# Kernel tuning notes

Measured on AMD Instinct MI355X. Metric: run time of the kernel, lower is better.

## Reference

```python
import jax, jax.numpy as jnp
import numpy as np

FEAT = 1152
HID = [768, 512, 256]
WS = 32
LN_EPS = 1e-5


def _ln(x, g, b):
    mu = jnp.mean(x, axis=-1, keepdims=True)
    var = jnp.mean(jnp.square(x - mu), axis=-1, keepdims=True)
    return (x - mu) * jax.lax.rsqrt(var + LN_EPS) * g + b


def setup_inputs() -> dict:
    key = jax.random.key(0)
    ks = jax.random.split(key, 16)
    B, N, C = 8, 9216, FEAT

    def lin(k, din, dout):
        s = 1.0 / np.sqrt(din)
        k1, k2 = jax.random.split(k)
        return (jax.random.uniform(k1, (din, dout), jnp.float32, -s, s),
                jax.random.uniform(k2, (dout,), jnp.float32, -s, s))

    x = jax.random.normal(ks[0], (B, N, C), jnp.float32)
    W1, b1 = lin(ks[1], C, HID[0])
    W2, b2 = lin(ks[2], HID[0], HID[1])
    W3, b3 = lin(ks[3], HID[1], HID[2])
    Wo, bo = lin(ks[4], HID[2], C)
    red = C // 8
    ca_w1, ca_b1 = lin(ks[5], C, red)
    ca_w2, ca_b2 = lin(ks[6], red, C)
    return {
        "x": x,
        "W1": W1, "b1": b1, "g1": jnp.ones((HID[0],)), "be1": jnp.zeros((HID[0],)),
        "W2": W2, "b2": b2, "g2": jnp.ones((HID[1],)), "be2": jnp.zeros((HID[1],)),
        "W3": W3, "b3": b3, "g3": jnp.ones((HID[2],)), "be3": jnp.zeros((HID[2],)),
        "Wo": Wo, "bo": bo,
        "ca_w1": ca_w1, "ca_b1": ca_b1, "ca_w2": ca_w2, "ca_b2": ca_b2,
    }


def reference(x, W1, b1, g1, be1, W2, b2, g2, be2, W3, b3, g3, be3,
              Wo, bo, ca_w1, ca_b1, ca_w2, ca_b2):
    B, N, C = x.shape
    # projection + hidden blocks: Linear -> GELU(exact) -> LayerNorm
    h = _ln(jax.nn.gelu(x @ W1 + b1, approximate=False), g1, be1)
    h = _ln(jax.nn.gelu(h @ W2 + b2, approximate=False), g2, be2)
    h = _ln(jax.nn.gelu(h @ W3 + b3, approximate=False), g3, be3)
    y = h @ Wo + bo  # (B, N, C)
    # SE channel attention: global avg-pool over seq, 1x1 convs (=linear)
    pooled = jnp.mean(y, axis=1)                                  # (B, C)
    s = jax.nn.relu(pooled @ ca_w1 + ca_b1)                       # (B, C/8)
    s = jax.nn.sigmoid(s @ ca_w2 + ca_b2)                         # (B, C)
    y = y * s[:, None, :]
    # block-diagonal local self-attention, window = WS, scale 1/sqrt(C)
    nw = N // WS
    yw = y.reshape(B, nw, WS, C)
    scores = jnp.einsum('bwqc,bwkc->bwqk', yw, yw) / jnp.sqrt(jnp.asarray(C, y.dtype))
    attn = jax.nn.softmax(scores, axis=-1)
    out = jnp.einsum('bwqk,bwkc->bwqc', attn, yw)
    return out.reshape(B, N, C)
```

## Files before the change

### kernel.cpp

```cpp
#include <hip/hip_runtime.h>
#include <cstdint>
#include <cstddef>

typedef __bf16 bf16;
typedef __bf16 bf16x8 __attribute__((ext_vector_type(8)));
typedef float f32x4 __attribute__((ext_vector_type(4)));

__device__ __forceinline__ void gload_lds16(const bf16* g, bf16* l) {
    __builtin_amdgcn_global_load_lds((const __attribute__((address_space(1))) void*)g,
                                     (__attribute__((address_space(3))) void*)l, 16, 0, 0);
}

__global__ void cvt_f32_bf16_kernel(const float* __restrict__ in, bf16* __restrict__ outp, size_t n) {
    const size_t i = ((size_t)blockIdx.x * 256 + threadIdx.x) * 8;
    if (i >= n) return;
    const float4 a = *(const float4*)(in + i);
    const float4 b = *(const float4*)(in + i + 4);
    bf16x8 o;
    o[0] = (bf16)a.x; o[1] = (bf16)a.y; o[2] = (bf16)a.z; o[3] = (bf16)a.w;
    o[4] = (bf16)b.x; o[5] = (bf16)b.y; o[6] = (bf16)b.z; o[7] = (bf16)b.w;
    *(bf16x8*)(outp + i) = o;
}

__global__ void wtrans_all_kernel(const float* __restrict__ W1, bf16* __restrict__ T1,
                                  const float* __restrict__ W2, bf16* __restrict__ T2,
                                  const float* __restrict__ W3, bf16* __restrict__ T3,
                                  const float* __restrict__ Wo, bf16* __restrict__ To)
{
    __shared__ bf16 tile[64][65];
    const int id = blockIdx.x;
    const int t = threadIdx.x;
    const float* W; bf16* T; int K, N, kb, nb;
    if (id < 216)      { W = W1; T = T1; K = 1152; N = 768;  const int r = id;       kb = r % 18; nb = r / 18; }
    else if (id < 312) { W = W2; T = T2; K = 768;  N = 512;  const int r = id - 216; kb = r % 12; nb = r / 12; }
    else if (id < 344) { W = W3; T = T3; K = 512;  N = 256;  const int r = id - 312; kb = r % 8;  nb = r / 8;  }
    else               { W = Wo; T = To; K = 256;  N = 1152; const int r = id - 344; kb = r % 4;  nb = r / 4;  }
    const int k0 = kb << 6;
    const int n0 = nb << 6;
#pragma unroll
    for (int i = 0; i < 16; ++i) {
        const int flat = i * 256 + t;
        const int r = flat >> 6;
        const int c = flat & 63;
        tile[c][r] = (bf16)W[(size_t)(k0 + r) * N + n0 + c];
    }
    __syncthreads();
#pragma unroll
    for (int i = 0; i < 16; ++i) {
        const int flat = i * 256 + t;
        const int r = flat >> 6;
        const int c = flat & 63;
        T[(size_t)(n0 + r) * K + k0 + c] = tile[r][c];
    }
}

__device__ __forceinline__ int xcd_swz(int bid, int nwg) {
    return (bid & 7) * (nwg >> 3) + (bid >> 3);
}

__global__ void gemm_bf16_kernel(const bf16* __restrict__ A, const bf16* __restrict__ Bt,
                                 const float* __restrict__ bias, bf16* __restrict__ C,
                                 int K, int N, int nx, int do_gelu,
                                 float* __restrict__ ppart)
{
    __shared__ bf16 Alds[128 * 64];
    __shared__ bf16 Blds[128 * 64];
    __shared__ float psum[2][128];
    const int t = threadIdx.x;
    const int w = t >> 6;
    const int l = t & 63;
    const int l15 = l & 15, l4 = l >> 4;
    const int wgid = xcd_swz(blockIdx.x, gridDim.x);
    const int mblk = wgid / nx;
    const int nblk = wgid - mblk * nx;
    const int m0 = mblk << 7;
    const int n0 = nblk << 7;
    const int wm = (w >> 1) << 6;
    const int wn = (w & 1) << 6;

    f32x4 acc[4][4] = {};

    int sr[4], sg[4];
#pragma unroll
    for (int i = 0; i < 4; ++i) {
        const int flat = i * 256 + t;
        sr[i] = flat >> 3;
        sg[i] = ((flat & 7) ^ (sr[i] & 7)) << 3;
    }

    for (int k0 = 0; k0 < K; k0 += 64) {
#pragma unroll
        for (int i = 0; i < 4; ++i) {
            gload_lds16(A + (size_t)(m0 + sr[i]) * K + (k0 + sg[i]),
                        &Alds[(size_t)(i * 256 + (w << 6)) << 3]);
            gload_lds16(Bt + (size_t)(n0 + sr[i]) * K + (k0 + sg[i]),
                        &Blds[(size_t)(i * 256 + (w << 6)) << 3]);
        }
        __syncthreads();
#pragma unroll
        for (int kk = 0; kk < 2; ++kk) {
            bf16x8 af[4], bfv[4];
#pragma unroll
            for (int i = 0; i < 4; ++i) {
                const int r = wm + (i << 4) + l15;
                const int g = (kk << 2) + l4;
                af[i] = *(const bf16x8*)&Alds[(r << 6) + ((g ^ (r & 7)) << 3)];
                const int rn = wn + (i << 4) + l15;
                bfv[i] = *(const bf16x8*)&Blds[(rn << 6) + ((g ^ (rn & 7)) << 3)];
            }
#pragma unroll
            for (int i = 0; i < 4; ++i)
#pragma unroll
                for (int j = 0; j < 4; ++j)
                    acc[i][j] = __builtin_amdgcn_mfma_f32_16x16x32_bf16(af[i], bfv[j], acc[i][j], 0, 0, 0);
        }
        __syncthreads();
    }

#pragma unroll
    for (int i = 0; i < 4; ++i) {
        const int mb = m0 + wm + (i << 4) + (l4 << 2);
#pragma unroll
        for (int j = 0; j < 4; ++j) {
            const int col = n0 + wn + (j << 4) + l15;
            const float bv = bias[col];
#pragma unroll
            for (int r = 0; r < 4; ++r) {
                float v = acc[i][j][r] + bv;
                if (do_gelu) v = 0.5f * v * (1.0f + erff(v * 0.70710678118654752f));
                C[(size_t)(mb + r) * N + col] = (bf16)v;
            }
        }
    }

    if (ppart) {
#pragma unroll
        for (int j = 0; j < 4; ++j) {
            float cs = 0.f;
#pragma unroll
            for (int i = 0; i < 4; ++i)
#pragma unroll
                for (int r = 0; r < 4; ++r) cs += acc[i][j][r];
            cs += __shfl_xor(cs, 16, 64);
            cs += __shfl_xor(cs, 32, 64);
            if (l4 == 0) psum[w >> 1][((w & 1) << 6) + (j << 4) + l15] = cs;
        }
        __syncthreads();
        if (t < 128) {
            const int col = n0 + t;
            ppart[(size_t)mblk * N + col] = psum[0][t] + psum[1][t] + 128.0f * bias[col];
        }
    }
}

__global__ void ln768_kernel(bf16* __restrict__ H, const float* __restrict__ g,
                             const float* __restrict__ be)
{
    const int t = threadIdx.x;
    const int rloc = t >> 7;
    const int u = t & 127;
    bf16* hp = H + ((size_t)blockIdx.x * 2 + rloc) * 768;
    float v[8];
    float s1 = 0.f, s2 = 0.f;
    if (u < 96) {
        const bf16x8 hv = *(const bf16x8*)(hp + u * 8);
#pragma unroll
        for (int e = 0; e < 8; ++e) { v[e] = (float)hv[e]; s1 += v[e]; s2 += v[e] * v[e]; }
    }
#pragma unroll
    for (int m = 1; m < 64; m <<= 1) { s1 += __shfl_xor(s1, m, 64); s2 += __shfl_xor(s2, m, 64); }
    __shared__ float red[8];
    const int w = t >> 6;
    if ((t & 63) == 0) { red[w] = s1; red[w + 4] = s2; }
    __syncthreads();
    const int wb = rloc << 1;
    s1 = red[wb] + red[wb + 1];
    s2 = red[wb + 4] + red[wb + 5];
    const float mu = s1 * (1.0f / 768.0f);
    const float rstd = rsqrtf(s2 * (1.0f / 768.0f) - mu * mu + 1e-5f);
    if (u < 96) {
        const float4 g0 = *(const float4*)(g + u * 8);
        const float4 g1 = *(const float4*)(g + u * 8 + 4);
        const float4 b0 = *(const float4*)(be + u * 8);
        const float4 b1 = *(const float4*)(be + u * 8 + 4);
        bf16x8 o;
        o[0] = (bf16)((v[0] - mu) * rstd * g0.x + b0.x);
        o[1] = (bf16)((v[1] - mu) * rstd * g0.y + b0.y);
        o[2] = (bf16)((v[2] - mu) * rstd * g0.z + b0.z);
        o[3] = (bf16)((v[3] - mu) * rstd * g0.w + b0.w);
        o[4] = (bf16)((v[4] - mu) * rstd * g1.x + b1.x);
        o[5] = (bf16)((v[5] - mu) * rstd * g1.y + b1.y);
        o[6] = (bf16)((v[6] - mu) * rstd * g1.z + b1.z);
        o[7] = (bf16)((v[7] - mu) * rstd * g1.w + b1.w);
        *(bf16x8*)(hp + u * 8) = o;
    }
}

__global__ void ln512_kernel(bf16* __restrict__ H, const float* __restrict__ g,
                             const float* __restrict__ be)
{
    const int t = threadIdx.x;
    const int w = t >> 6, l = t & 63;
    bf16* hp = H + ((size_t)blockIdx.x * 4 + w) * 512;
    const bf16x8 hv = *(const bf16x8*)(hp + l * 8);
    float v[8];
    float s1 = 0.f, s2 = 0.f;
#pragma unroll
    for (int e = 0; e < 8; ++e) { v[e] = (float)hv[e]; s1 += v[e]; s2 += v[e] * v[e]; }
#pragma unroll
    for (int m = 1; m < 64; m <<= 1) { s1 += __shfl_xor(s1, m, 64); s2 += __shfl_xor(s2, m, 64); }
    const float mu = s1 * (1.0f / 512.0f);
    const float rstd = rsqrtf(s2 * (1.0f / 512.0f) - mu * mu + 1e-5f);
    const float4 g0 = *(const float4*)(g + l * 8);
    const float4 g1 = *(const float4*)(g + l * 8 + 4);
    const float4 b0 = *(const float4*)(be + l * 8);
    const float4 b1 = *(const float4*)(be + l * 8 + 4);
    bf16x8 o;
    o[0] = (bf16)((v[0] - mu) * rstd * g0.x + b0.x);
    o[1] = (bf16)((v[1] - mu) * rstd * g0.y + b0.y);
    o[2] = (bf16)((v[2] - mu) * rstd * g0.z + b0.z);
    o[3] = (bf16)((v[3] - mu) * rstd * g0.w + b0.w);
    o[4] = (bf16)((v[4] - mu) * rstd * g1.x + b1.x);
    o[5] = (bf16)((v[5] - mu) * rstd * g1.y + b1.y);
    o[6] = (bf16)((v[6] - mu) * rstd * g1.z + b1.z);
    o[7] = (bf16)((v[7] - mu) * rstd * g1.w + b1.w);
    *(bf16x8*)(hp + l * 8) = o;
}

__global__ void ln256_kernel(bf16* __restrict__ H, const float* __restrict__ g,
                             const float* __restrict__ be)
{
    const int t = threadIdx.x;
    const int rloc = t >> 5, l = t & 31;
    bf16* hp = H + ((size_t)blockIdx.x * 8 + rloc) * 256;
    const bf16x8 hv = *(const bf16x8*)(hp + l * 8);
    float v[8];
    float s1 = 0.f, s2 = 0.f;
#pragma unroll
    for (int e = 0; e < 8; ++e) { v[e] = (float)hv[e]; s1 += v[e]; s2 += v[e] * v[e]; }
#pragma unroll
    for (int m = 1; m < 32; m <<= 1) { s1 += __shfl_xor(s1, m, 64); s2 += __shfl_xor(s2, m, 64); }
    const float mu = s1 * (1.0f / 256.0f);
    const float rstd = rsqrtf(s2 * (1.0f / 256.0f) - mu * mu + 1e-5f);
    const float4 g0 = *(const float4*)(g + l * 8);
    const float4 g1 = *(const float4*)(g + l * 8 + 4);
    const float4 b0 = *(const float4*)(be + l * 8);
    const float4 b1 = *(const float4*)(be + l * 8 + 4);
    bf16x8 o;
    o[0] = (bf16)((v[0] - mu) * rstd * g0.x + b0.x);
    o[1] = (bf16)((v[1] - mu) * rstd * g0.y + b0.y);
    o[2] = (bf16)((v[2] - mu) * rstd * g0.z + b0.z);
    o[3] = (bf16)((v[3] - mu) * rstd * g0.w + b0.w);
    o[4] = (bf16)((v[4] - mu) * rstd * g1.x + b1.x);
    o[5] = (bf16)((v[5] - mu) * rstd * g1.y + b1.y);
    o[6] = (bf16)((v[6] - mu) * rstd * g1.z + b1.z);
    o[7] = (bf16)((v[7] - mu) * rstd * g1.w + b1.w);
    *(bf16x8*)(hp + l * 8) = o;
}

__global__ void se_kernel(const float* __restrict__ ppart,
                          const float* __restrict__ w1, const float* __restrict__ b1,
                          const float* __restrict__ w2, const float* __restrict__ b2,
                          float* __restrict__ sbuf)
{
    const int b = blockIdx.x, t = threadIdx.x;
    __shared__ float p[1152];
    __shared__ float t1[144];
    for (int c = t; c < 1152; c += 256) {
        float s = 0.f;
#pragma unroll 8
        for (int j = 0; j < 72; ++j) s += ppart[(size_t)(b * 72 + j) * 1152 + c];
        p[c] = s * (1.0f / 9216.0f);
    }
    __syncthreads();
    if (t < 144) {
        float a = b1[t];
        for (int k = 0; k < 1152; ++k) a += p[k] * w1[k * 144 + t];
        t1[t] = a > 0.f ? a : 0.f;
    }
    __syncthreads();
    for (int c = t; c < 1152; c += 256) {
        float a = b2[c];
#pragma unroll 8
        for (int k = 0; k < 144; ++k) a += t1[k] * w2[k * 1152 + c];
        sbuf[b * 1152 + c] = 1.0f / (1.0f + expf(-a));
    }
}

__device__ __forceinline__ int fswz(int r) { return (r & 7) ^ ((r >> 3) & 3); }

#define OSTG_STRIDE 388

__global__ void attn_kernel(const bf16* __restrict__ Y, const float* __restrict__ sbuf,
                            float* __restrict__ out)
{
    __shared__ __align__(16) char smem[24576 + 24832 + 2048];
    bf16*  yw   = (bf16*)smem;
    float* SpF  = (float*)(smem + 24576);
    float* ostg = (float*)(smem + 24576);
    bf16*  P    = (bf16*)(smem + 24576 + 24832);

    const int t = threadIdx.x;
    const int w = t >> 6, l = t & 63;
    const int l15 = l & 15, l4 = l >> 4;
    const int wdx = blockIdx.x, b = blockIdx.y;

    const bf16* Yp = Y + ((size_t)b * 9216 + (size_t)wdx * 32) * 1152;
    const float* sv = sbuf + b * 1152;
    float* op = out + ((size_t)b * 9216 + (size_t)wdx * 32) * 1152;

    auto stage_chunk = [&](int cc) {
#pragma unroll
        for (int i = 0; i < 6; ++i) {
            const int flat = i * 256 + t;
            const int r = flat / 48;
            const int gg = flat - r * 48;
            const int c0 = cc * 384 + gg * 8;
            const bf16x8 yv = *(const bf16x8*)(Yp + (size_t)r * 1152 + c0);
            const float4 sa = *(const float4*)(sv + c0);
            const float4 sb = *(const float4*)(sv + c0 + 4);
            bf16x8 ov;
            ov[0] = (bf16)((float)yv[0] * sa.x);
            ov[1] = (bf16)((float)yv[1] * sa.y);
            ov[2] = (bf16)((float)yv[2] * sa.z);
            ov[3] = (bf16)((float)yv[3] * sa.w);
            ov[4] = (bf16)((float)yv[4] * sb.x);
            ov[5] = (bf16)((float)yv[5] * sb.y);
            ov[6] = (bf16)((float)yv[6] * sb.z);
            ov[7] = (bf16)((float)yv[7] * sb.w);
            *(bf16x8*)&yw[((r * 48) + (gg ^ fswz(r))) << 3] = ov;
        }
    };

    f32x4 acc[2][2] = {};
    for (int cc = 0; cc < 3; ++cc) {
        if (cc) __syncthreads();
        stage_chunk(cc);
        __syncthreads();
#pragma unroll
        for (int kkl = 0; kkl < 3; ++kkl) {
            const int g = ((w * 3 + kkl) << 2) + l4;
            bf16x8 af[2];
#pragma unroll
            for (int i = 0; i < 2; ++i) {
                const int r = (i << 4) + l15;
                af[i] = *(const bf16x8*)&yw[((r * 48) + (g ^ fswz(r))) << 3];
            }
#pragma unroll
            for (int i = 0; i < 2; ++i)
#pragma unroll
                for (int j = 0; j < 2; ++j)
                    acc[i][j] = __builtin_amdgcn_mfma_f32_16x16x32_bf16(af[i], af[j], acc[i][j], 0, 0, 0);
        }
    }
#pragma unroll
    for (int i = 0; i < 2; ++i)
#pragma unroll
        for (int j = 0; j < 2; ++j)
#pragma unroll
            for (int r = 0; r < 4; ++r)
                SpF[w * 1056 + ((i << 4) + (l4 << 2) + r) * 33 + (j << 4) + l15] = acc[i][j][r];
    __syncthreads();

    {
        const int q = t >> 3, u = t & 7;
        float v[4];
#pragma unroll
        for (int e = 0; e < 4; ++e) {
            const int k2 = (u << 2) + e;
            v[e] = (SpF[q * 33 + k2] + SpF[1056 + q * 33 + k2] +
                    SpF[2112 + q * 33 + k2] + SpF[3168 + q * 33 + k2]) * 0.029462782549439483f;
        }
        float mx = fmaxf(fmaxf(v[0], v[1]), fmaxf(v[2], v[3]));
#pragma unroll
        for (int m = 1; m < 8; m <<= 1) mx = fmaxf(mx, __shfl_xor(mx, m, 64));
        float sm = 0.f;
#pragma unroll
        for (int e = 0; e < 4; ++e) { v[e] = expf(v[e] - mx); sm += v[e]; }
#pragma unroll
        for (int m = 1; m < 8; m <<= 1) sm += __shfl_xor(sm, m, 64);
        const float inv = 1.0f / sm;
#pragma unroll
        for (int e = 0; e < 4; ++e) P[(q << 5) + (u << 2) + e] = (bf16)(v[e] * inv);
    }
    __syncthreads();

    bf16x8 pa[2];
#pragma unroll
    for (int i = 0; i < 2; ++i)
        pa[i] = *(const bf16x8*)&P[(((i << 4) + l15) << 5) + (l4 << 3)];

    for (int ci = 0; ci < 3; ++ci) {
        const int cc = (ci == 0) ? 2 : (ci - 1);
        if (ci) {
            __syncthreads();
            stage_chunk(cc);
            __syncthreads();
        }
        f32x4 pacc[2][6] = {};
#pragma unroll
        for (int jn = 0; jn < 6; ++jn) {
            const int nl = w * 96 + (jn << 4) + l15;
            const int gg = nl >> 3, e = nl & 7;
            bf16x8 bv;
#pragma unroll
            for (int j = 0; j < 8; ++j) {
                const int kr = (l4 << 3) + j;
                bv[j] = yw[(((kr * 48) + (gg ^ fswz(kr))) << 3) + e];
            }
#pragma unroll
            for (int i = 0; i < 2; ++i)
                pacc[i][jn] = __builtin_amdgcn_mfma_f32_16x16x32_bf16(pa[i], bv, pacc[i][jn], 0, 0, 0);
        }
#pragma unroll
        for (int half = 0; half < 2; ++half) {
            if (half) __syncthreads();
#pragma unroll
            for (int jn = 0; jn < 6; ++jn)
#pragma unroll
                for (int r = 0; r < 4; ++r)
                    ostg[((l4 << 2) + r) * OSTG_STRIDE + w * 96 + (jn << 4) + l15] =
                        pacc[half][jn][r];
            __syncthreads();
            {
                const int row = t >> 4;
                const int cb = (t & 15) << 2;
                float* orow = op + (size_t)(row + (half << 4)) * 1152 + cc * 384;
                const float* srow = &ostg[row * OSTG_STRIDE];
#pragma unroll
                for (int k2 = 0; k2 < 6; ++k2) {
                    const int c = cb + (k2 << 6);
                    *(float4*)(orow + c) = *(const float4*)(srow + c);
                }
            }
        }
        if (ci < 2) __syncthreads();
    }
}

extern "C" void kernel_launch(void* const* d_in, const int* in_sizes, int n_in,
                              void* d_out, int out_size, void* d_ws, size_t ws_size,
                              hipStream_t stream)
{
    const float* x   = (const float*)d_in[0];
    const float* W1  = (const float*)d_in[1];
    const float* b1  = (const float*)d_in[2];
    const float* g1  = (const float*)d_in[3];
    const float* be1 = (const float*)d_in[4];
    const float* W2  = (const float*)d_in[5];
    const float* b2  = (const float*)d_in[6];
    const float* g2  = (const float*)d_in[7];
    const float* be2 = (const float*)d_in[8];
    const float* W3  = (const float*)d_in[9];
    const float* b3  = (const float*)d_in[10];
    const float* g3  = (const float*)d_in[11];
    const float* be3 = (const float*)d_in[12];
    const float* Wo  = (const float*)d_in[13];
    const float* bo  = (const float*)d_in[14];
    const float* cw1 = (const float*)d_in[15];
    const float* cb1 = (const float*)d_in[16];
    const float* cw2 = (const float*)d_in[17];
    const float* cb2 = (const float*)d_in[18];
    float* out = (float*)d_out;

    const int M = 8 * 9216;
    size_t off = 0;
    auto alloc = [&](size_t nbytes) {
        void* p = (char*)d_ws + off;
        off += (nbytes + 255) & ~(size_t)255;
        return p;
    };
    bf16* Yb  = (bf16*)alloc((size_t)M * 1152 * 2);
    bf16* Hb  = (bf16*)alloc((size_t)M * 768 * 2);
    bf16* H2  = (bf16*)alloc((size_t)M * 512 * 2);
    bf16* Wt1 = (bf16*)alloc(768ull * 1152 * 2);
    bf16* Wt2 = (bf16*)alloc(512ull * 768 * 2);
    bf16* Wt3 = (bf16*)alloc(256ull * 512 * 2);
    bf16* Wto = (bf16*)alloc(1152ull * 256 * 2);
    float* ppart = (float*)alloc(576ull * 1152 * 4);
    float* sbuf  = (float*)alloc(8ull * 1152 * 4);
    bf16* Xb = Yb;
    bf16* H1 = Hb;
    bf16* H3 = Hb;

    cvt_f32_bf16_kernel<<<41472, 256, 0, stream>>>(x, Xb, (size_t)M * 1152);
    wtrans_all_kernel<<<416, 256, 0, stream>>>(W1, Wt1, W2, Wt2, W3, Wt3, Wo, Wto);

    gemm_bf16_kernel<<<6 * 576, 256, 0, stream>>>(Xb, Wt1, b1, H1, 1152, 768, 6, 1, nullptr);
    ln768_kernel<<<M / 2, 256, 0, stream>>>(H1, g1, be1);
    gemm_bf16_kernel<<<4 * 576, 256, 0, stream>>>(H1, Wt2, b2, H2, 768, 512, 4, 1, nullptr);
    ln512_kernel<<<M / 4, 256, 0, stream>>>(H2, g2, be2);
    gemm_bf16_kernel<<<2 * 576, 256, 0, stream>>>(H2, Wt3, b3, H3, 512, 256, 2, 1, nullptr);
    ln256_kernel<<<M / 8, 256, 0, stream>>>(H3, g3, be3);
    gemm_bf16_kernel<<<9 * 576, 256, 0, stream>>>(H3, Wto, bo, Yb, 256, 1152, 9, 0, ppart);

    se_kernel<<<8, 256, 0, stream>>>(ppart, cw1, cb1, cw2, cb2, sbuf);
    attn_kernel<<<dim3(288, 8), 256, 0, stream>>>(Yb, sbuf, out);
}
```

Measured before the change: 822.0 us.

## Fuse fp32-to-bf16 input conversion into first GEMM's LDS load path

Removes the standalone conversion kernel and has the first GEMM stage fp32 activations into LDS with a swizzled layout, converting to bf16 when building MFMA fragments. This avoids a full write and re-read of the converted input. In exchange the first GEMM loads twice the A bytes per tile, repeated across column blocks, and uses more LDS, which may lower occupancy. The GEMM is also split into specialized variants for the plain and pooling epilogues, removing runtime branches.

```diff
diff --git a/kernel.cpp b/kernel.cpp
--- a/kernel.cpp
+++ b/kernel.cpp
@@ -10,16 +10,9 @@
     __builtin_amdgcn_global_load_lds((const __attribute__((address_space(1))) void*)g,
                                      (__attribute__((address_space(3))) void*)l, 16, 0, 0);
 }
-
-__global__ void cvt_f32_bf16_kernel(const float* __restrict__ in, bf16* __restrict__ outp, size_t n) {
-    const size_t i = ((size_t)blockIdx.x * 256 + threadIdx.x) * 8;
-    if (i >= n) return;
-    const float4 a = *(const float4*)(in + i);
-    const float4 b = *(const float4*)(in + i + 4);
-    bf16x8 o;
-    o[0] = (bf16)a.x; o[1] = (bf16)a.y; o[2] = (bf16)a.z; o[3] = (bf16)a.w;
-    o[4] = (bf16)b.x; o[5] = (bf16)b.y; o[6] = (bf16)b.z; o[7] = (bf16)b.w;
-    *(bf16x8*)(outp + i) = o;
+__device__ __forceinline__ void gload_lds16f(const float* g, float* l) {
+    __builtin_amdgcn_global_load_lds((const __attribute__((address_space(1))) void*)g,
+                                     (__attribute__((address_space(3))) void*)l, 16, 0, 0);
 }
 
 __global__ void wtrans_all_kernel(const float* __restrict__ W1, bf16* __restrict__ T1,
@@ -58,14 +51,12 @@
     return (bid & 7) * (nwg >> 3) + (bid >> 3);
 }
 
-__global__ void gemm_bf16_kernel(const bf16* __restrict__ A, const bf16* __restrict__ Bt,
+__global__ void gemm_f32a_kernel(const float* __restrict__ A, const bf16* __restrict__ Bt,
                                  const float* __restrict__ bias, bf16* __restrict__ C,
-                                 int K, int N, int nx, int do_gelu,
-                                 float* __restrict__ ppart)
-{
-    __shared__ bf16 Alds[128 * 64];
-    __shared__ bf16 Blds[128 * 64];
-    __shared__ float psum[2][128];
+                                 int K, int N, int nx)
+{
+    __shared__ float Af32[128 * 64];
+    __shared__ bf16  Blds[128 * 64];
     const int t = threadIdx.x;
     const int w = t >> 6;
     const int l = t & 63;
@@ -80,6 +71,94 @@
 
     f32x4 acc[4][4] = {};
 
+    int ar[8], ag[8];
+#pragma unroll
+    for (int i = 0; i < 8; ++i) {
+        const int flat = i * 256 + t;
+        ar[i] = flat >> 4;
+        ag[i] = ((flat & 15) ^ (ar[i] & 15)) << 2;
+    }
+    int br[4], bg[4];
+#pragma unroll
+    for (int i = 0; i < 4; ++i) {
+        const int flat = i * 256 + t;
+        br[i] = flat >> 3;
+        bg[i] = ((flat & 7) ^ (br[i] & 7)) << 3;
+    }
+
+    for (int k0 = 0; k0 < K; k0 += 64) {
+#pragma unroll
+        for (int i = 0; i < 8; ++i)
+            gload_lds16f(A + (size_t)(m0 + ar[i]) * K + (k0 + ag[i]),
+                         &Af32[(i * 256 + (w << 6)) << 2]);
+#pragma unroll
+        for (int i = 0; i < 4; ++i)
+            gload_lds16(Bt + (size_t)(n0 + br[i]) * K + (k0 + bg[i]),
+                        &Blds[(i * 256 + (w << 6)) << 3]);
+        __syncthreads();
+#pragma unroll
+        for (int kk = 0; kk < 2; ++kk) {
+            bf16x8 af[4], bfv[4];
+#pragma unroll
+            for (int i = 0; i < 4; ++i) {
+                const int r = wm + (i << 4) + l15;
+                const int s2 = (((kk << 2) + l4) << 1);
+                const float4 fa = *(const float4*)&Af32[(r << 6) + ((s2 ^ (r & 15)) << 2)];
+                const float4 fb = *(const float4*)&Af32[(r << 6) + (((s2 + 1) ^ (r & 15)) << 2)];
+                bf16x8 a;
+                a[0] = (bf16)fa.x; a[1] = (bf16)fa.y; a[2] = (bf16)fa.z; a[3] = (bf16)fa.w;
+                a[4] = (bf16)fb.x; a[5] = (bf16)fb.y; a[6] = (bf16)fb.z; a[7] = (bf16)fb.w;
+                af[i] = a;
+                const int rn = wn + (i << 4) + l15;
+                const int g = (kk << 2) + l4;
+                bfv[i] = *(const bf16x8*)&Blds[(rn << 6) + ((g ^ (rn & 7)) << 3)];
+            }
+#pragma unroll
+            for (int i = 0; i < 4; ++i)
+#pragma unroll
+                for (int j = 0; j < 4; ++j)
+                    acc[i][j] = __builtin_amdgcn_mfma_f32_16x16x32_bf16(af[i], bfv[j], acc[i][j], 0, 0, 0);
+        }
+        __syncthreads();
+    }
+
+#pragma unroll
+    for (int i = 0; i < 4; ++i) {
+        const int mb = m0 + wm + (i << 4) + (l4 << 2);
+#pragma unroll
+        for (int j = 0; j < 4; ++j) {
+            const int col = n0 + wn + (j << 4) + l15;
+            const float bv = bias[col];
+#pragma unroll
+            for (int r = 0; r < 4; ++r) {
+                float v = acc[i][j][r] + bv;
+                v = 0.5f * v * (1.0f + erff(v * 0.70710678118654752f));
+                C[(size_t)(mb + r) * N + col] = (bf16)v;
+            }
+        }
+    }
+}
+
+__global__ void gemm_bf16_kernel(const bf16* __restrict__ A, const bf16* __restrict__ Bt,
+                                 const float* __restrict__ bias, bf16* __restrict__ C,
+                                 int K, int N, int nx, int do_gelu)
+{
+    __shared__ bf16 Alds[128 * 64];
+    __shared__ bf16 Blds[128 * 64];
+    const int t = threadIdx.x;
+    const int w = t >> 6;
+    const int l = t & 63;
+    const int l15 = l & 15, l4 = l >> 4;
+    const int wgid = xcd_swz(blockIdx.x, gridDim.x);
+    const int mblk = wgid / nx;
+    const int nblk = wgid - mblk * nx;
+    const int m0 = mblk << 7;
+    const int n0 = nblk << 7;
+    const int wm = (w >> 1) << 6;
+    const int wn = (w & 1) << 6;
+
+    f32x4 acc[4][4] = {};
+
     int sr[4], sg[4];
 #pragma unroll
     for (int i = 0; i < 4; ++i) {
@@ -132,24 +211,94 @@
             }
         }
     }
-
-    if (ppart) {
+}
+
+__global__ void gemm_pool_kernel(const bf16* __restrict__ A, const bf16* __restrict__ Bt,
+                                 const float* __restrict__ bias, bf16* __restrict__ C,
+                                 int K, int N, int nx, float* __restrict__ ppart)
+{
+    __shared__ bf16 Alds[128 * 64];
+    __shared__ bf16 Blds[128 * 64];
+    __shared__ float psum[2][128];
+    const int t = threadIdx.x;
+    const int w = t >> 6;
+    const int l = t & 63;
+    const int l15 = l & 15, l4 = l >> 4;
+    const int wgid = xcd_swz(blockIdx.x, gridDim.x);
+    const int mblk = wgid / nx;
+    const int nblk = wgid - mblk * nx;
+    const int m0 = mblk << 7;
+    const int n0 = nblk << 7;
+    const int wm = (w >> 1) << 6;
+    const int wn = (w & 1) << 6;
+
+    f32x4 acc[4][4] = {};
+
+    int sr[4], sg[4];
+#pragma unroll
+    for (int i = 0; i < 4; ++i) {
+        const int flat = i * 256 + t;
+        sr[i] = flat >> 3;
+        sg[i] = ((flat & 7) ^ (sr[i] & 7)) << 3;
+    }
+
+    for (int k0 = 0; k0 < K; k0 += 64) {
+#pragma unroll
+        for (int i = 0; i < 4; ++i) {
+            gload_lds16(A + (size_t)(m0 + sr[i]) * K + (k0 + sg[i]),
+                        &Alds[(size_t)(i * 256 + (w << 6)) << 3]);
+            gload_lds16(Bt + (size_t)(n0 + sr[i]) * K + (k0 + sg[i]),
+                        &Blds[(size_t)(i * 256 + (w << 6)) << 3]);
+        }
+        __syncthreads();
+#pragma unroll
+        for (int kk = 0; kk < 2; ++kk) {
+            bf16x8 af[4], bfv[4];
+#pragma unroll
+            for (int i = 0; i < 4; ++i) {
+                const int r = wm + (i << 4) + l15;
+                const int g = (kk << 2) + l4;
+                af[i] = *(const bf16x8*)&Alds[(r << 6) + ((g ^ (r & 7)) << 3)];
+                const int rn = wn + (i << 4) + l15;
+                bfv[i] = *(const bf16x8*)&Blds[(rn << 6) + ((g ^ (rn & 7)) << 3)];
+            }
+#pragma unroll
+            for (int i = 0; i < 4; ++i)
+#pragma unroll
+                for (int j = 0; j < 4; ++j)
+                    acc[i][j] = __builtin_amdgcn_mfma_f32_16x16x32_bf16(af[i], bfv[j], acc[i][j], 0, 0, 0);
+        }
+        __syncthreads();
+    }
+
+#pragma unroll
+    for (int i = 0; i < 4; ++i) {
+        const int mb = m0 + wm + (i << 4) + (l4 << 2);
 #pragma unroll
         for (int j = 0; j < 4; ++j) {
-            float cs = 0.f;
-#pragma unroll
-            for (int i = 0; i < 4; ++i)
-#pragma unroll
-                for (int r = 0; r < 4; ++r) cs += acc[i][j][r];
-            cs += __shfl_xor(cs, 16, 64);
-            cs += __shfl_xor(cs, 32, 64);
-            if (l4 == 0) psum[w >> 1][((w & 1) << 6) + (j << 4) + l15] = cs;
-        }
-        __syncthreads();
-        if (t < 128) {
-            const int col = n0 + t;
-            ppart[(size_t)mblk * N + col] = psum[0][t] + psum[1][t] + 128.0f * bias[col];
-        }
+            const int col = n0 + wn + (j << 4) + l15;
+            const float bv = bias[col];
+#pragma unroll
+            for (int r = 0; r < 4; ++r)
+                C[(size_t)(mb + r) * N + col] = (bf16)(acc[i][j][r] + bv);
+        }
+    }
+
+#pragma unroll
+    for (int j = 0; j < 4; ++j) {
+        float cs = 0.f;
+#pragma unroll
+        for (int i = 0; i < 4; ++i)
+#pragma unroll
+            for (int r = 0; r < 4; ++r) cs += acc[i][j][r];
+        cs += __shfl_xor(cs, 16, 64);
+        cs += __shfl_xor(cs, 32, 64);
+        if (l4 == 0) psum[w >> 1][((w & 1) << 6) + (j << 4) + l15] = cs;
+    }
+    __syncthreads();
+    if (t < 128) {
+        const int col = n0 + t;
+        ppart[(size_t)mblk * N + col] = psum[0][t] + psum[1][t] + 128.0f * bias[col];
     }
 }
 
@@ -479,20 +628,18 @@
     bf16* Wto = (bf16*)alloc(1152ull * 256 * 2);
     float* ppart = (float*)alloc(576ull * 1152 * 4);
     float* sbuf  = (float*)alloc(8ull * 1152 * 4);
-    bf16* Xb = Yb;
     bf16* H1 = Hb;
     bf16* H3 = Hb;
 
-    cvt_f32_bf16_kernel<<<41472, 256, 0, stream>>>(x, Xb, (size_t)M * 1152);
     wtrans_all_kernel<<<416, 256, 0, stream>>>(W1, Wt1, W2, Wt2, W3, Wt3, Wo, Wto);
 
-    gemm_bf16_kernel<<<6 * 576, 256, 0, stream>>>(Xb, Wt1, b1, H1, 1152, 768, 6, 1, nullptr);
+    gemm_f32a_kernel<<<6 * 576, 256, 0, stream>>>(x, Wt1, b1, H1, 1152, 768, 6);
     ln768_kernel<<<M / 2, 256, 0, stream>>>(H1, g1, be1);
-    gemm_bf16_kernel<<<4 * 576, 256, 0, stream>>>(H1, Wt2, b2, H2, 768, 512, 4, 1, nullptr);
+    gemm_bf16_kernel<<<4 * 576, 256, 0, stream>>>(H1, Wt2, b2, H2, 768, 512, 4, 1);
     ln512_kernel<<<M / 4, 256, 0, stream>>>(H2, g2, be2);
-    gemm_bf16_kernel<<<2 * 576, 256, 0, stream>>>(H2, Wt3, b3, H3, 512, 256, 2, 1, nullptr);
+    gemm_bf16_kernel<<<2 * 576, 256, 0, stream>>>(H2, Wt3, b3, H3, 512, 256, 2, 1);
     ln256_kernel<<<M / 8, 256, 0, stream>>>(H3, g3, be3);
-    gemm_bf16_kernel<<<9 * 576, 256, 0, stream>>>(H3, Wto, bo, Yb, 256, 1152, 9, 0, ppart);
+    gemm_pool_kernel<<<9 * 576, 256, 0, stream>>>(H3, Wto, bo, Yb, 256, 1152, 9, ppart);
 
     se_kernel<<<8, 256, 0, stream>>>(ppart, cw1, cb1, cw2, cb2, sbuf);
     attn_kernel<<<dim3(288, 8), 256, 0, stream>>>(Yb, sbuf, out);
```

Result: faster. 804.7 us (-2.1%).
